# Kernel tuning notes

Measured on AMD Instinct MI355X. Metric: run time of the kernel, lower is better.

## Reference

```python
import jax, jax.numpy as jnp
import numpy as np
from jax import lax

SIGMA = 1.5
KERNEL_SIZE = 11
C1 = 0.01 ** 2  # (k1 * data_range)^2 with data_range = 1.0
C2 = 0.03 ** 2


def _gaussian_kernel_1d(kernel_size: int, sigma: float) -> jnp.ndarray:
    coords = jnp.arange(kernel_size, dtype=jnp.float32) - (kernel_size - 1) / 2.0
    g = jnp.exp(-(coords ** 2) / (2.0 * sigma ** 2))
    return g / jnp.sum(g)


def _gaussian_blur(x: jnp.ndarray, g: jnp.ndarray) -> jnp.ndarray:
    """Separable depthwise Gaussian blur, VALID padding. x: [B,C,H,W], g: [k]."""
    c = x.shape[1]
    k = g.shape[0]
    dn = lax.conv_dimension_numbers(x.shape, (c, 1, k, 1), ('NCHW', 'OIHW', 'NCHW'))
    wh = jnp.broadcast_to(g.reshape(1, 1, k, 1), (c, 1, k, 1)).astype(x.dtype)
    ww = jnp.broadcast_to(g.reshape(1, 1, 1, k), (c, 1, 1, k)).astype(x.dtype)
    y = lax.conv_general_dilated(x, wh, (1, 1), 'VALID', dimension_numbers=dn, feature_group_count=c)
    y = lax.conv_general_dilated(y, ww, (1, 1), 'VALID', dimension_numbers=dn, feature_group_count=c)
    return y


def setup_inputs() -> dict:
    key = jax.random.key(0)
    k1, k2 = jax.random.split(key)
    shape = (16, 3, 512, 512)
    return {
        'input': jax.random.uniform(k1, shape, dtype=jnp.float32),
        'target': jax.random.uniform(k2, shape, dtype=jnp.float32),
    }


def reference(input, target):
    g = _gaussian_kernel_1d(KERNEL_SIZE, SIGMA)
    mu_x = _gaussian_blur(input, g)
    mu_y = _gaussian_blur(target, g)
    mu_x2 = mu_x * mu_x
    mu_y2 = mu_y * mu_y
    mu_xy = mu_x * mu_y
    var_x = _gaussian_blur(input * input, g) - mu_x2
    var_y = _gaussian_blur(target * target, g) - mu_y2
    cov_xy = _gaussian_blur(input * target, g) - mu_xy
    ssim_map = ((2.0 * mu_xy + C1) * (2.0 * cov_xy + C2)) / ((mu_x2 + mu_y2 + C1) * (var_x + var_y + C2))
    return 1.0 - jnp.mean(ssim_map)
```

## Files before the change

### kernel.cpp

```cpp
#include <hip/hip_runtime.h>

#define IH 512
#define IW 512
#define OH 502
#define OW 502
#define KS 11
#define HO 16
#define NSTRIP 32
#define NCH 48
#define NBLK (NCH * NSTRIP)
#define NT 256
#define LROW 528
#define C1f 0.0001f
#define C2f 0.0009f

__device__ __constant__ float g_w[KS] = {
    0.00102838f, 0.00759876f, 0.03600077f, 0.10936069f, 0.21300554f,
    0.26601173f, 0.21300554f, 0.10936069f, 0.03600077f, 0.00759876f,
    0.00102838f};

#define BARRIER() do {                                        \
    asm volatile("s_waitcnt lgkmcnt(0)" ::: "memory");        \
    __builtin_amdgcn_s_barrier();                             \
} while (0)

__global__ __launch_bounds__(NT, 1) void ssim_main(const float* __restrict__ x,
                                                   const float* __restrict__ y,
                                                   double* __restrict__ acc,
                                                   unsigned int* __restrict__ cnt,
                                                   float* __restrict__ out) {
    __shared__ float lds[5][2][LROW];
    __shared__ float red[4];

    const int t = threadIdx.x;
    const int ch = blockIdx.x / NSTRIP;
    const int strip = blockIdx.x % NSTRIP;
    const int r0 = strip * HO;
    const float* __restrict__ xc = x + (size_t)ch * IH * IW + 2 * t;
    const float* __restrict__ yc = y + (size_t)ch * IH * IW + 2 * t;

    float2 rx[12], ry[12];
#pragma unroll
    for (int i = 0; i < 12; ++i) {
        const int gr = min(r0 + i, IH - 1);
        rx[i] = *(const float2*)(xc + gr * IW);
        ry[i] = *(const float2*)(yc + gr * IW);
    }
    float2 nx0, ny0, nx1, ny1;
    {
        const int g0 = min(r0 + 12, IH - 1);
        const int g1 = min(r0 + 13, IH - 1);
        nx0 = *(const float2*)(xc + g0 * IW);
        ny0 = *(const float2*)(yc + g0 * IW);
        nx1 = *(const float2*)(xc + g1 * IW);
        ny1 = *(const float2*)(yc + g1 * IW);
    }

    float lsum = 0.f;

    for (int k = 0; k < HO / 2; ++k) {
#pragma unroll
        for (int rr = 0; rr < 2; ++rr) {
            float s0[2] = {0.f, 0.f}, s1[2] = {0.f, 0.f}, s2[2] = {0.f, 0.f};
            float s3[2] = {0.f, 0.f}, s4[2] = {0.f, 0.f};
#pragma unroll
            for (int tp = 0; tp < KS; ++tp) {
                const float w = g_w[tp];
                const float2 xv = rx[rr + tp];
                const float2 yv = ry[rr + tp];
                const float wx0 = w * xv.x, wx1 = w * xv.y;
                const float wy0 = w * yv.x, wy1 = w * yv.y;
                s0[0] += wx0;  s0[1] += wx1;
                s1[0] += wy0;  s1[1] += wy1;
                s2[0] = fmaf(wx0, xv.x, s2[0]);  s2[1] = fmaf(wx1, xv.y, s2[1]);
                s3[0] = fmaf(wy0, yv.x, s3[0]);  s3[1] = fmaf(wy1, yv.y, s3[1]);
                s4[0] = fmaf(wx0, yv.x, s4[0]);  s4[1] = fmaf(wx1, yv.y, s4[1]);
            }
            *(float2*)&lds[0][rr][2 * t] = make_float2(s0[0], s0[1]);
            *(float2*)&lds[1][rr][2 * t] = make_float2(s1[0], s1[1]);
            *(float2*)&lds[2][rr][2 * t] = make_float2(s2[0], s2[1]);
            *(float2*)&lds[3][rr][2 * t] = make_float2(s3[0], s3[1]);
            *(float2*)&lds[4][rr][2 * t] = make_float2(s4[0], s4[1]);
        }
        BARRIER();

        {
            const int rr = t >> 7;
            const int c4 = (t & 127) * 4;
            const int orow = r0 + 2 * k + rr;
            float m[5][4];
#pragma unroll
            for (int q = 0; q < 5; ++q) {
                float f[16];
#pragma unroll
                for (int a = 0; a < 4; ++a)
                    *(float4*)&f[4 * a] = *(const float4*)&lds[q][rr][c4 + 4 * a];
#pragma unroll
                for (int cc = 0; cc < 4; ++cc) {
                    float s = 0.f;
#pragma unroll
                    for (int tp = 0; tp < KS; ++tp) s = fmaf(g_w[tp], f[cc + tp], s);
                    m[q][cc] = s;
                }
            }
            if (orow < OH) {
#pragma unroll
                for (int cc = 0; cc < 4; ++cc) {
                    const int gc = c4 + cc;
                    if (gc < OW) {
                        const float mux2 = m[0][cc] * m[0][cc];
                        const float muy2 = m[1][cc] * m[1][cc];
                        const float muxy = m[0][cc] * m[1][cc];
                        const float vx = m[2][cc] - mux2;
                        const float vy = m[3][cc] - muy2;
                        const float cxy = m[4][cc] - muxy;
                        const float num = (2.f * muxy + C1f) * (2.f * cxy + C2f);
                        const float den = (mux2 + muy2 + C1f) * (vx + vy + C2f);
                        float r = __builtin_amdgcn_rcpf(den);
                        r = r * fmaf(-den, r, 2.0f);
                        lsum = fmaf(num, r, lsum);
                    }
                }
            }
        }

#pragma unroll
        for (int i = 0; i < 10; ++i) { rx[i] = rx[i + 2]; ry[i] = ry[i + 2]; }
        rx[10] = nx0; ry[10] = ny0;
        rx[11] = nx1; ry[11] = ny1;

        {
            const int g0 = min(r0 + 2 * k + 14, IH - 1);
            const int g1 = min(r0 + 2 * k + 15, IH - 1);
            nx0 = *(const float2*)(xc + g0 * IW);
            ny0 = *(const float2*)(yc + g0 * IW);
            nx1 = *(const float2*)(xc + g1 * IW);
            ny1 = *(const float2*)(yc + g1 * IW);
        }
        BARRIER();
    }

#pragma unroll
    for (int off = 32; off > 0; off >>= 1) lsum += __shfl_down(lsum, off, 64);
    const int wave = t >> 6, lane = t & 63;
    if (lane == 0) red[wave] = lsum;
    __syncthreads();
    if (t == 0) {
        const float bs = (red[0] + red[1]) + (red[2] + red[3]);
        atomicAdd(acc, (double)bs);
        __threadfence();
        const unsigned int prev = atomicAdd(cnt, 1u);
        if (prev == (unsigned int)(NBLK - 1)) {
            const double total = atomicAdd(acc, 0.0);
            out[0] = (float)(1.0 - total / 12096192.0);
        }
    }
}

extern "C" void kernel_launch(void* const* d_in, const int* in_sizes, int n_in,
                              void* d_out, int out_size, void* d_ws, size_t ws_size,
                              hipStream_t stream) {
    const float* x = (const float*)d_in[0];
    const float* y = (const float*)d_in[1];
    float* out = (float*)d_out;
    double* acc = (double*)d_ws;
    unsigned int* cnt = (unsigned int*)((char*)d_ws + 8);

    hipMemsetAsync(d_ws, 0, 16, stream);
    ssim_main<<<NBLK, NT, 0, stream>>>(x, y, acc, cnt, out);
}
```

Before: 90.79 us.

## Process two row strips per block with ping-pong LDS to overlap vertical and horizontal blur

Each block now handles two 16-row strips (A and B) of the same channel and alternates between them. The vertical blur of one strip is interleaved with the horizontal blur of the other through double-buffered LDS. This halves the block count and lets VALU work and LDS reads from independent strips hide each other's latency across barriers. The cost is higher register pressure from two row windows and the prefetch registers, and fewer blocks to spread over the CUs.

```diff
diff --git a/kernel.cpp b/kernel.cpp
--- a/kernel.cpp
+++ b/kernel.cpp
@@ -6,9 +6,9 @@
 #define OW 502
 #define KS 11
 #define HO 16
-#define NSTRIP 32
+#define NPAIR 16
 #define NCH 48
-#define NBLK (NCH * NSTRIP)
+#define NBLK (NCH * NPAIR)
 #define NT 256
 #define LROW 528
 #define C1f 0.0001f
@@ -23,122 +23,152 @@
     asm volatile("s_waitcnt lgkmcnt(0)" ::: "memory");        \
     __builtin_amdgcn_s_barrier();                             \
 } while (0)
+
+#define VBLUR(RX, RY, NX0, NY0, SI)                                           \
+    {                                                                         \
+        float s0[2]={0,0}, s1[2]={0,0}, s2[2]={0,0}, s3[2]={0,0}, s4[2]={0,0};\
+        _Pragma("unroll")                                                     \
+        for (int tp = 0; tp < KS; ++tp) {                                     \
+            const float w = g_w[tp];                                          \
+            const float2 xv = RX[tp], yv = RY[tp];                            \
+            const float wx0 = w*xv.x, wx1 = w*xv.y;                           \
+            const float wy0 = w*yv.x, wy1 = w*yv.y;                           \
+            s0[0]+=wx0; s0[1]+=wx1; s1[0]+=wy0; s1[1]+=wy1;                   \
+            s2[0]=fmaf(wx0,xv.x,s2[0]); s2[1]=fmaf(wx1,xv.y,s2[1]);           \
+            s3[0]=fmaf(wy0,yv.x,s3[0]); s3[1]=fmaf(wy1,yv.y,s3[1]);           \
+            s4[0]=fmaf(wx0,yv.x,s4[0]); s4[1]=fmaf(wx1,yv.y,s4[1]);           \
+        }                                                                     \
+        *(float2*)&lds[SI][0][0][2*t] = make_float2(s0[0], s0[1]);            \
+        *(float2*)&lds[SI][1][0][2*t] = make_float2(s1[0], s1[1]);            \
+        *(float2*)&lds[SI][2][0][2*t] = make_float2(s2[0], s2[1]);            \
+        *(float2*)&lds[SI][3][0][2*t] = make_float2(s3[0], s3[1]);            \
+        *(float2*)&lds[SI][4][0][2*t] = make_float2(s4[0], s4[1]);            \
+        float u0[2]={0,0}, u1[2]={0,0}, u2[2]={0,0}, u3[2]={0,0}, u4[2]={0,0};\
+        _Pragma("unroll")                                                     \
+        for (int tp = 0; tp < KS; ++tp) {                                     \
+            const float w = g_w[tp];                                          \
+            const float2 xv = (tp < KS-1) ? RX[tp+1] : NX0;                   \
+            const float2 yv = (tp < KS-1) ? RY[tp+1] : NY0;                   \
+            const float wx0 = w*xv.x, wx1 = w*xv.y;                           \
+            const float wy0 = w*yv.x, wy1 = w*yv.y;                           \
+            u0[0]+=wx0; u0[1]+=wx1; u1[0]+=wy0; u1[1]+=wy1;                   \
+            u2[0]=fmaf(wx0,xv.x,u2[0]); u2[1]=fmaf(wx1,xv.y,u2[1]);           \
+            u3[0]=fmaf(wy0,yv.x,u3[0]); u3[1]=fmaf(wy1,yv.y,u3[1]);           \
+            u4[0]=fmaf(wx0,yv.x,u4[0]); u4[1]=fmaf(wx1,yv.y,u4[1]);           \
+        }                                                                     \
+        *(float2*)&lds[SI][0][1][2*t] = make_float2(u0[0], u0[1]);            \
+        *(float2*)&lds[SI][1][1][2*t] = make_float2(u1[0], u1[1]);            \
+        *(float2*)&lds[SI][2][1][2*t] = make_float2(u2[0], u2[1]);            \
+        *(float2*)&lds[SI][3][1][2*t] = make_float2(u3[0], u3[1]);            \
+        *(float2*)&lds[SI][4][1][2*t] = make_float2(u4[0], u4[1]);            \
+    }
+
+#define SHIFTPREF(RX, RY, NX0, NY0, NX1, NY1, R0, KK)                         \
+    {                                                                         \
+        _Pragma("unroll")                                                     \
+        for (int i = 0; i < KS-2; ++i) { RX[i]=RX[i+2]; RY[i]=RY[i+2]; }      \
+        RX[KS-2]=NX0; RY[KS-2]=NY0; RX[KS-1]=NX1; RY[KS-1]=NY1;               \
+        const int g0 = min((R0)+2*(KK)+13, IH-1);                             \
+        const int g1 = min((R0)+2*(KK)+14, IH-1);                             \
+        NX0 = *(const float2*)(xc + g0*IW); NY0 = *(const float2*)(yc + g0*IW);\
+        NX1 = *(const float2*)(xc + g1*IW); NY1 = *(const float2*)(yc + g1*IW);\
+    }
+
+#define HBLUR(SI, R0, KK)                                                     \
+    {                                                                         \
+        const int rr = t >> 7;                                                \
+        const int c4 = (t & 127) * 4;                                         \
+        const int orow = (R0) + 2*(KK) + rr;                                  \
+        float m[5][4];                                                        \
+        _Pragma("unroll")                                                     \
+        for (int q = 0; q < 5; ++q) {                                         \
+            float f[16];                                                      \
+            _Pragma("unroll")                                                 \
+            for (int a = 0; a < 4; ++a)                                       \
+                *(float4*)&f[4*a] = *(const float4*)&lds[SI][q][rr][c4+4*a];  \
+            _Pragma("unroll")                                                 \
+            for (int cc = 0; cc < 4; ++cc) {                                  \
+                float s = 0.f;                                                \
+                _Pragma("unroll")                                             \
+                for (int tp = 0; tp < KS; ++tp)                               \
+                    s = fmaf(g_w[tp], f[cc+tp], s);                           \
+                m[q][cc] = s;                                                 \
+            }                                                                 \
+        }                                                                     \
+        if (orow < OH) {                                                      \
+            _Pragma("unroll")                                                 \
+            for (int cc = 0; cc < 4; ++cc) {                                  \
+                const int gc = c4 + cc;                                       \
+                if (gc < OW) {                                                \
+                    const float mux2 = m[0][cc]*m[0][cc];                     \
+                    const float muy2 = m[1][cc]*m[1][cc];                     \
+                    const float muxy = m[0][cc]*m[1][cc];                     \
+                    const float vx = m[2][cc] - mux2;                         \
+                    const float vy = m[3][cc] - muy2;                         \
+                    const float cxy = m[4][cc] - muxy;                        \
+                    const float num = (2.f*muxy + C1f) * (2.f*cxy + C2f);     \
+                    const float den = (mux2 + muy2 + C1f) * (vx + vy + C2f);  \
+                    float r_ = __builtin_amdgcn_rcpf(den);                    \
+                    r_ = r_ * fmaf(-den, r_, 2.0f);          \
+                    lsum = fmaf(num, r_, lsum);                               \
+                }                                                             \
+            }                                                                 \
+        }                                                                     \
+    }
 
 __global__ __launch_bounds__(NT, 1) void ssim_main(const float* __restrict__ x,
                                                    const float* __restrict__ y,
                                                    double* __restrict__ acc,
                                                    unsigned int* __restrict__ cnt,
                                                    float* __restrict__ out) {
-    __shared__ float lds[5][2][LROW];
+    __shared__ float lds[2][5][2][LROW];
     __shared__ float red[4];
 
     const int t = threadIdx.x;
-    const int ch = blockIdx.x / NSTRIP;
-    const int strip = blockIdx.x % NSTRIP;
-    const int r0 = strip * HO;
+    const int ch = blockIdx.x / NPAIR;
+    const int pr = blockIdx.x % NPAIR;
+    const int r0A = pr * HO;
+    const int r0B = (pr + NPAIR) * HO;
     const float* __restrict__ xc = x + (size_t)ch * IH * IW + 2 * t;
     const float* __restrict__ yc = y + (size_t)ch * IH * IW + 2 * t;
 
-    float2 rx[12], ry[12];
+    float2 rxA[KS], ryA[KS], rxB[KS], ryB[KS];
 #pragma unroll
-    for (int i = 0; i < 12; ++i) {
-        const int gr = min(r0 + i, IH - 1);
-        rx[i] = *(const float2*)(xc + gr * IW);
-        ry[i] = *(const float2*)(yc + gr * IW);
-    }
-    float2 nx0, ny0, nx1, ny1;
-    {
-        const int g0 = min(r0 + 12, IH - 1);
-        const int g1 = min(r0 + 13, IH - 1);
-        nx0 = *(const float2*)(xc + g0 * IW);
-        ny0 = *(const float2*)(yc + g0 * IW);
-        nx1 = *(const float2*)(xc + g1 * IW);
-        ny1 = *(const float2*)(yc + g1 * IW);
-    }
+    for (int i = 0; i < KS; ++i) {
+        rxA[i] = *(const float2*)(xc + min(r0A + i, IH-1) * IW);
+        ryA[i] = *(const float2*)(yc + min(r0A + i, IH-1) * IW);
+        rxB[i] = *(const float2*)(xc + min(r0B + i, IH-1) * IW);
+        ryB[i] = *(const float2*)(yc + min(r0B + i, IH-1) * IW);
+    }
+    float2 nxA0, nyA0, nxA1, nyA1, nxB0, nyB0, nxB1, nyB1;
+    nxA0 = *(const float2*)(xc + min(r0A+11, IH-1)*IW);
+    nyA0 = *(const float2*)(yc + min(r0A+11, IH-1)*IW);
+    nxA1 = *(const float2*)(xc + min(r0A+12, IH-1)*IW);
+    nyA1 = *(const float2*)(yc + min(r0A+12, IH-1)*IW);
+    nxB0 = *(const float2*)(xc + min(r0B+11, IH-1)*IW);
+    nyB0 = *(const float2*)(yc + min(r0B+11, IH-1)*IW);
+    nxB1 = *(const float2*)(xc + min(r0B+12, IH-1)*IW);
+    nyB1 = *(const float2*)(yc + min(r0B+12, IH-1)*IW);
 
     float lsum = 0.f;
 
-    for (int k = 0; k < HO / 2; ++k) {
-#pragma unroll
-        for (int rr = 0; rr < 2; ++rr) {
-            float s0[2] = {0.f, 0.f}, s1[2] = {0.f, 0.f}, s2[2] = {0.f, 0.f};
-            float s3[2] = {0.f, 0.f}, s4[2] = {0.f, 0.f};
-#pragma unroll
-            for (int tp = 0; tp < KS; ++tp) {
-                const float w = g_w[tp];
-                const float2 xv = rx[rr + tp];
-                const float2 yv = ry[rr + tp];
-                const float wx0 = w * xv.x, wx1 = w * xv.y;
-                const float wy0 = w * yv.x, wy1 = w * yv.y;
-                s0[0] += wx0;  s0[1] += wx1;
-                s1[0] += wy0;  s1[1] += wy1;
-                s2[0] = fmaf(wx0, xv.x, s2[0]);  s2[1] = fmaf(wx1, xv.y, s2[1]);
-                s3[0] = fmaf(wy0, yv.x, s3[0]);  s3[1] = fmaf(wy1, yv.y, s3[1]);
-                s4[0] = fmaf(wx0, yv.x, s4[0]);  s4[1] = fmaf(wx1, yv.y, s4[1]);
-            }
-            *(float2*)&lds[0][rr][2 * t] = make_float2(s0[0], s0[1]);
-            *(float2*)&lds[1][rr][2 * t] = make_float2(s1[0], s1[1]);
-            *(float2*)&lds[2][rr][2 * t] = make_float2(s2[0], s2[1]);
-            *(float2*)&lds[3][rr][2 * t] = make_float2(s3[0], s3[1]);
-            *(float2*)&lds[4][rr][2 * t] = make_float2(s4[0], s4[1]);
-        }
+    VBLUR(rxA, ryA, nxA0, nyA0, 0);
+    SHIFTPREF(rxA, ryA, nxA0, nyA0, nxA1, nyA1, r0A, 0);
+    BARRIER();
+    for (int k = 0; k < 7; ++k) {
+        VBLUR(rxB, ryB, nxB0, nyB0, 1);
+        SHIFTPREF(rxB, ryB, nxB0, nyB0, nxB1, nyB1, r0B, k);
+        HBLUR(0, r0A, k);
         BARRIER();
-
-        {
-            const int rr = t >> 7;
-            const int c4 = (t & 127) * 4;
-            const int orow = r0 + 2 * k + rr;
-            float m[5][4];
-#pragma unroll
-            for (int q = 0; q < 5; ++q) {
-                float f[16];
-#pragma unroll
-                for (int a = 0; a < 4; ++a)
-                    *(float4*)&f[4 * a] = *(const float4*)&lds[q][rr][c4 + 4 * a];
-#pragma unroll
-                for (int cc = 0; cc < 4; ++cc) {
-                    float s = 0.f;
-#pragma unroll
-                    for (int tp = 0; tp < KS; ++tp) s = fmaf(g_w[tp], f[cc + tp], s);
-                    m[q][cc] = s;
-                }
-            }
-            if (orow < OH) {
-#pragma unroll
-                for (int cc = 0; cc < 4; ++cc) {
-                    const int gc = c4 + cc;
-                    if (gc < OW) {
-                        const float mux2 = m[0][cc] * m[0][cc];
-                        const float muy2 = m[1][cc] * m[1][cc];
-                        const float muxy = m[0][cc] * m[1][cc];
-                        const float vx = m[2][cc] - mux2;
-                        const float vy = m[3][cc] - muy2;
-                        const float cxy = m[4][cc] - muxy;
-                        const float num = (2.f * muxy + C1f) * (2.f * cxy + C2f);
-                        const float den = (mux2 + muy2 + C1f) * (vx + vy + C2f);
-                        float r = __builtin_amdgcn_rcpf(den);
-                        r = r * fmaf(-den, r, 2.0f);
-                        lsum = fmaf(num, r, lsum);
-                    }
-                }
-            }
-        }
-
-#pragma unroll
-        for (int i = 0; i < 10; ++i) { rx[i] = rx[i + 2]; ry[i] = ry[i + 2]; }
-        rx[10] = nx0; ry[10] = ny0;
-        rx[11] = nx1; ry[11] = ny1;
-
-        {
-            const int g0 = min(r0 + 2 * k + 14, IH - 1);
-            const int g1 = min(r0 + 2 * k + 15, IH - 1);
-            nx0 = *(const float2*)(xc + g0 * IW);
-            ny0 = *(const float2*)(yc + g0 * IW);
-            nx1 = *(const float2*)(xc + g1 * IW);
-            ny1 = *(const float2*)(yc + g1 * IW);
-        }
+        VBLUR(rxA, ryA, nxA0, nyA0, 0);
+        SHIFTPREF(rxA, ryA, nxA0, nyA0, nxA1, nyA1, r0A, k + 1);
+        HBLUR(1, r0B, k);
         BARRIER();
     }
+    VBLUR(rxB, ryB, nxB0, nyB0, 1);
+    HBLUR(0, r0A, 7);
+    BARRIER();
+    HBLUR(1, r0B, 7);
 
 #pragma unroll
     for (int off = 32; off > 0; off >>= 1) lsum += __shfl_down(lsum, off, 64);
```

Result: no change. 91.18 us (+0.4%).
